# Optimization experiments

Hardware: AMD Instinct MI355X
Metric: run time of the kernel (lower is better)

Reference implementation:

```python
import jax, jax.numpy as jnp
import numpy as np


def sign_fn(x):
    # torch.sign(torch.sign(x) + 0.5): maps x >= 0 -> +1, x < 0 -> -1 (zero -> +1)
    return jnp.where(x >= 0, 1.0, -1.0).astype(x.dtype)


def setup_inputs() -> dict:
    key = jax.random.key(0)
    kx, kw, kb = jax.random.split(key, 3)
    TOKENS, IN, OUT = 8192, 4096, 4096
    x = jax.random.normal(kx, (TOKENS, IN), dtype=jnp.float32)
    weight = jax.random.normal(kw, (OUT, IN), dtype=jnp.float32)
    bias = jax.random.normal(kb, (OUT,), dtype=jnp.float32)
    return {"x": x, "weight": weight, "bias": bias}


def reference(x, weight, bias):
    b_weight = sign_fn(weight)  # [out, in], values in {+1, -1}
    b_bias = sign_fn(bias)      # [out]
    # nn.functional.linear: y = x @ W^T + b
    return jnp.einsum('ti,oi->to', x, b_weight) + b_bias
```

## Files before the change

### kernel.cpp

```cpp
#include <hip/hip_runtime.h>


typedef __attribute__((ext_vector_type(4))) int   i32x4;
typedef __attribute__((ext_vector_type(8))) short short8;
typedef __attribute__((ext_vector_type(4))) float f32x4;

constexpr int M = 8192;
constexpr int N = 4096;
constexpr int K = 4096;

constexpr int BM = 256, BN = 256, BK = 64;
constexpr int NTILES = K / BK;
constexpr int TILE_A = BM * BK;
constexpr int TILE_B = BN * BK;
constexpr int BUFSZ  = TILE_A + TILE_B;
constexpr int RING   = 4;

__device__ __forceinline__ void load_lds16(const void* g, void* l) {
    __builtin_amdgcn_global_load_lds(
        (const __attribute__((address_space(1))) unsigned int*)g,
        (__attribute__((address_space(3))) unsigned int*)l, 16, 0, 0);
}

constexpr int WB  = 1024;
constexpr int WCH = N * K / 8;

__global__ __launch_bounds__(256) void prep_fused(
    const float* __restrict__ X, const float* __restrict__ W,
    signed char* __restrict__ Xq, signed char* __restrict__ Wq,
    float* __restrict__ Scale) {
    __shared__ float wmax[4];
    const int t = threadIdx.x;

    if (blockIdx.x < M) {
        const int row = blockIdx.x;
        const float4* xr = reinterpret_cast<const float4*>(X + (size_t)row * K);
        float4 v[4];
        float mx = 0.f;
#pragma unroll
        for (int i = 0; i < 4; ++i) {
            v[i] = xr[t + i * 256];
            mx = fmaxf(mx, fmaxf(fmaxf(fabsf(v[i].x), fabsf(v[i].y)),
                                 fmaxf(fabsf(v[i].z), fabsf(v[i].w))));
        }
#pragma unroll
        for (int off = 32; off > 0; off >>= 1)
            mx = fmaxf(mx, __shfl_down(mx, off));
        if ((t & 63) == 0) wmax[t >> 6] = mx;
        __syncthreads();
        float rmax = fmaxf(fmaxf(wmax[0], wmax[1]), fmaxf(wmax[2], wmax[3]));
        rmax = fmaxf(rmax, 1e-20f);
        const float inv = 127.f / rmax;
        if (t == 0) Scale[row] = rmax * (1.f / 127.f);

        unsigned int* out = reinterpret_cast<unsigned int*>(Xq + (size_t)row * K);
#pragma unroll
        for (int i = 0; i < 4; ++i) {
            int q0 = (int)rintf(v[i].x * inv);
            int q1 = (int)rintf(v[i].y * inv);
            int q2 = (int)rintf(v[i].z * inv);
            int q3 = (int)rintf(v[i].w * inv);
            unsigned int p = (q0 & 255) | ((q1 & 255) << 8) |
                             ((q2 & 255) << 16) | ((unsigned)(q3 & 255) << 24);
            out[t + i * 256] = p;
        }
    } else {
        const float4* W4 = reinterpret_cast<const float4*>(W);
        uint2* O = reinterpret_cast<uint2*>(Wq);
        auto sg = [](float f) -> unsigned int { return (f >= 0.f) ? 1u : 0xFFu; };
        size_t idx = (size_t)(blockIdx.x - M) * 256 + t;
        const size_t stride = (size_t)WB * 256;
        for (size_t c = idx; c < (size_t)WCH; c += stride) {
            float4 a = W4[c * 2], b = W4[c * 2 + 1];
            uint2 o;
            o.x = sg(a.x) | (sg(a.y) << 8) | (sg(a.z) << 16) | (sg(a.w) << 24);
            o.y = sg(b.x) | (sg(b.y) << 8) | (sg(b.z) << 16) | (sg(b.w) << 24);
            O[c] = o;
        }
    }
}

struct GemmCtx {
    const signed char* Abase;
    const signed char* Bbase;
    int voff;
    signed char* lbase;
    unsigned baseA;
    unsigned baseB;
};

struct Frags { i32x4 b[4]; i32x4 a[8]; };

__device__ __forceinline__ void stage_full(const GemmCtx& c, int t) {
    signed char* d = c.lbase + (t & (RING - 1)) * BUFSZ;
    const size_t ko = (size_t)t * BK;
    load_lds16(c.Abase + ko + c.voff, d);
    load_lds16(c.Abase + (size_t)128 * K + ko + c.voff, d + 8192);
    load_lds16(c.Bbase + ko + c.voff, d + TILE_A);
    load_lds16(c.Bbase + (size_t)128 * K + ko + c.voff, d + TILE_A + 8192);
}

__device__ __forceinline__ void read_frags_asm(unsigned aA, unsigned aB,
                                               Frags& f) {
    asm volatile(
        "ds_read_b128 %0, %12 offset:0\n\t"
        "ds_read_b128 %1, %12 offset:1024\n\t"
        "ds_read_b128 %2, %12 offset:2048\n\t"
        "ds_read_b128 %3, %12 offset:3072\n\t"
        "ds_read_b128 %4, %13 offset:0\n\t"
        "ds_read_b128 %5, %13 offset:1024\n\t"
        "ds_read_b128 %6, %13 offset:2048\n\t"
        "ds_read_b128 %7, %13 offset:3072\n\t"
        "ds_read_b128 %8, %13 offset:4096\n\t"
        "ds_read_b128 %9, %13 offset:5120\n\t"
        "ds_read_b128 %10, %13 offset:6144\n\t"
        "ds_read_b128 %11, %13 offset:7168"
        : "=&v"(f.b[0]), "=&v"(f.b[1]), "=&v"(f.b[2]), "=&v"(f.b[3]),
          "=&v"(f.a[0]), "=&v"(f.a[1]), "=&v"(f.a[2]), "=&v"(f.a[3]),
          "=&v"(f.a[4]), "=&v"(f.a[5]), "=&v"(f.a[6]), "=&v"(f.a[7])
        : "v"(aB), "v"(aA));
}

__device__ __forceinline__ void do_mfma(const Frags& f, i32x4 (&acc)[8][4]) {
    __builtin_amdgcn_s_setprio(1);
#pragma unroll
    for (int mi = 0; mi < 8; ++mi)
#pragma unroll
        for (int ni = 0; ni < 4; ++ni)
            acc[mi][ni] = __builtin_amdgcn_mfma_i32_16x16x64_i8(
                f.a[mi], f.b[ni], acc[mi][ni], 0, 0, 0);
    __builtin_amdgcn_s_setprio(0);
}

template <int VM, bool STAGE, bool RDNEXT, bool BAR>
__device__ __forceinline__ void kstep(
    const GemmCtx& c, int j, Frags& cur, Frags& nxt, i32x4 (&acc)[8][4]) {
    if constexpr (RDNEXT) {
        const unsigned ring = (unsigned)(((j + 1) & (RING - 1)) * BUFSZ);
        read_frags_asm(c.baseA + ring, c.baseB + ring, nxt);
    }
    __builtin_amdgcn_sched_barrier(0);
    do_mfma(cur, acc);
    if constexpr (STAGE) stage_full(c, j + 4);
    if constexpr (VM >= 0)
        asm volatile("s_waitcnt vmcnt(%0)" :: "i"(VM) : "memory");
    asm volatile("s_waitcnt lgkmcnt(0)" ::: "memory");
    __builtin_amdgcn_sched_barrier(0);
    if constexpr (BAR) __builtin_amdgcn_s_barrier();
}

__global__ __launch_bounds__(512, 2) void gemm_i8_p(
    const signed char* __restrict__ Aq, const signed char* __restrict__ Bq,
    const float* __restrict__ Scale, const float* __restrict__ Bias,
    float* __restrict__ OUT) {
    __shared__ signed char smem[RING * BUFSZ];

    const int tid  = threadIdx.x;
    const int lane = tid & 63;
    const int w    = tid >> 6;
    const int wm   = w >> 2;
    const int wn   = w & 3;
    const int rl   = lane & 15;
    const int cq16 = (((lane >> 4) ^ ((rl >> 1) & 3)) << 4);

    const int wg  = blockIdx.x;
    const int lin = (wg & 7) * 64 + (wg >> 3);
    const int n0  = (lin & 15) * BN;
    const int m0  = (lin >> 4) * BM;

    const int srow = tid >> 2;
    const int cg   = ((tid & 3) ^ ((srow >> 1) & 3)) * 16;

    GemmCtx c;
    c.Abase = Aq + (size_t)m0 * K;
    c.Bbase = Bq + (size_t)n0 * K;
    c.voff  = srow * K + cg;
    c.lbase = smem + w * 1024;
    const unsigned lds0 = (unsigned)(unsigned long long)&smem[0];
    c.baseA = lds0 + (unsigned)((wm * 128 + rl) * BK + cq16);
    c.baseB = lds0 + (unsigned)(TILE_A + (wn * 64 + rl) * BK + cq16);

    i32x4 acc[8][4];
#pragma unroll
    for (int mi = 0; mi < 8; ++mi)
#pragma unroll
        for (int ni = 0; ni < 4; ++ni)
            acc[mi][ni] = (i32x4){0, 0, 0, 0};

    stage_full(c, 0); stage_full(c, 1); stage_full(c, 2); stage_full(c, 3);
    asm volatile("s_waitcnt vmcnt(8)" ::: "memory");
    __builtin_amdgcn_s_barrier();
    Frags fA, fB;
    read_frags_asm(c.baseA, c.baseB, fA);
    asm volatile("s_waitcnt lgkmcnt(0)" ::: "memory");
    __builtin_amdgcn_sched_barrier(0);
    __builtin_amdgcn_s_barrier();

    for (int j = 0; j < NTILES - 4; j += 2) {
        kstep<8, true, true, true>(c, j,     fA, fB, acc);
        kstep<8, true, true, true>(c, j + 1, fB, fA, acc);
    }
    kstep<4,  false, true,  true >(c, NTILES - 4, fA, fB, acc);
    kstep<0,  false, true,  true >(c, NTILES - 3, fB, fA, acc);
    kstep<-1, false, true,  false>(c, NTILES - 2, fA, fB, acc);
    kstep<-1, false, false, false>(c, NTILES - 1, fB, fA, acc);

#pragma unroll
    for (int ni = 0; ni < 4; ++ni) {
        const int gcol = n0 + wn * 64 + ni * 16 + rl;
        const float sb = (Bias[gcol] >= 0.f) ? 1.f : -1.f;
#pragma unroll
        for (int mi = 0; mi < 8; ++mi) {
            const int growb = m0 + wm * 128 + mi * 16 + (lane >> 4) * 4;
            const float4 sc = *reinterpret_cast<const float4*>(&Scale[growb]);
            OUT[(size_t)(growb + 0) * N + gcol] = (float)acc[mi][ni][0] * sc.x + sb;
            OUT[(size_t)(growb + 1) * N + gcol] = (float)acc[mi][ni][1] * sc.y + sb;
            OUT[(size_t)(growb + 2) * N + gcol] = (float)acc[mi][ni][2] * sc.z + sb;
            OUT[(size_t)(growb + 3) * N + gcol] = (float)acc[mi][ni][3] * sc.w + sb;
        }
    }
}

constexpr int MT   = 128;
constexpr int NTF  = 128;
constexpr int LDSS = 40;
constexpr int KTB  = 32;
__device__ __forceinline__ unsigned short f2b(float f) {
    unsigned int u = __builtin_bit_cast(unsigned int, f);
    u += 0x7FFFu + ((u >> 16) & 1u);
    return (unsigned short)(u >> 16);
}
__global__ __launch_bounds__(256) void binlin_fallback(
    const float* __restrict__ X, const float* __restrict__ W,
    const float* __restrict__ B, float* __restrict__ OUT) {
    __shared__ unsigned short As[MT][LDSS];
    __shared__ unsigned short Bs[NTF][LDSS];
    const int tid  = threadIdx.x;
    const int lane = tid & 63;
    const int wave = tid >> 6;
    const int wm   = wave >> 1;
    const int wn   = wave & 1;
    const int m0 = blockIdx.y * MT;
    const int n0 = blockIdx.x * NTF;
    const int rl = lane & 15;
    const int kq = (lane >> 4) * 8;
    f32x4 acc[4][4];
#pragma unroll
    for (int mi = 0; mi < 4; ++mi)
#pragma unroll
        for (int ni = 0; ni < 4; ++ni)
            acc[mi][ni] = (f32x4){0.f, 0.f, 0.f, 0.f};
    for (int k0 = 0; k0 < K; k0 += KTB) {
#pragma unroll
        for (int it = 0; it < 4; ++it) {
            int g = tid + it * 256, row = g >> 3, c4 = (g & 7) << 2;
            float4 v = *reinterpret_cast<const float4*>(&X[(size_t)(m0 + row) * K + k0 + c4]);
            ushort4 h;
            h.x = f2b(v.x); h.y = f2b(v.y); h.z = f2b(v.z); h.w = f2b(v.w);
            *reinterpret_cast<ushort4*>(&As[row][c4]) = h;
        }
#pragma unroll
        for (int it = 0; it < 4; ++it) {
            int g = tid + it * 256, row = g >> 3, c4 = (g & 7) << 2;
            float4 v = *reinterpret_cast<const float4*>(&W[(size_t)(n0 + row) * K + k0 + c4]);
            ushort4 h;
            h.x = (v.x >= 0.f) ? 0x3F80u : 0xBF80u;
            h.y = (v.y >= 0.f) ? 0x3F80u : 0xBF80u;
            h.z = (v.z >= 0.f) ? 0x3F80u : 0xBF80u;
            h.w = (v.w >= 0.f) ? 0x3F80u : 0xBF80u;
            *reinterpret_cast<ushort4*>(&Bs[row][c4]) = h;
        }
        __syncthreads();
        short8 a[4], b[4];
#pragma unroll
        for (int mi = 0; mi < 4; ++mi)
            a[mi] = *reinterpret_cast<const short8*>(&As[wm * 64 + mi * 16 + rl][kq]);
#pragma unroll
        for (int ni = 0; ni < 4; ++ni)
            b[ni] = *reinterpret_cast<const short8*>(&Bs[wn * 64 + ni * 16 + rl][kq]);
#pragma unroll
        for (int mi = 0; mi < 4; ++mi)
#pragma unroll
            for (int ni = 0; ni < 4; ++ni)
                acc[mi][ni] = __builtin_amdgcn_mfma_f32_16x16x32_bf16(
                    a[mi], b[ni], acc[mi][ni], 0, 0, 0);
        __syncthreads();
    }
#pragma unroll
    for (int ni = 0; ni < 4; ++ni) {
        int gcol = n0 + wn * 64 + ni * 16 + rl;
        float sb = (B[gcol] >= 0.f) ? 1.f : -1.f;
#pragma unroll
        for (int mi = 0; mi < 4; ++mi) {
            int growb = m0 + wm * 64 + mi * 16 + (lane >> 4) * 4;
#pragma unroll
            for (int r = 0; r < 4; ++r)
                OUT[(size_t)(growb + r) * N + gcol] = acc[mi][ni][r] + sb;
        }
    }
}

extern "C" void kernel_launch(void* const* d_in, const int* in_sizes, int n_in,
                              void* d_out, int out_size, void* d_ws, size_t ws_size,
                              hipStream_t stream) {
    const float* x  = (const float*)d_in[0];
    const float* w  = (const float*)d_in[1];
    const float* b  = (const float*)d_in[2];
    float* out      = (float*)d_out;

    const size_t need = (size_t)M * K + (size_t)N * K + (size_t)M * sizeof(float);
    if (ws_size >= need) {
        signed char* Xq = (signed char*)d_ws;
        signed char* Wq = Xq + (size_t)M * K;
        float* Scale    = (float*)(Wq + (size_t)N * K);

        prep_fused<<<dim3(M + WB), dim3(256), 0, stream>>>(x, w, Xq, Wq, Scale);
        gemm_i8_p<<<dim3((M / BM) * (N / BN)), dim3(512), 0, stream>>>(
            Xq, Wq, Scale, b, out);
    } else {
        dim3 grid(N / NTF, M / MT);
        binlin_fallback<<<grid, dim3(256), 0, stream>>>(x, w, b, out);
    }
}
```

Baseline: 402.5 us.

## Shrink GEMM tile to 128x256 with 4 waves and 3-slot LDS ring

Halves the M tile to 128 and uses 256-thread blocks (4 waves, each covering all 128 rows and 64 columns), doubling the grid. The LDS ring drops from 4 to 3 slots, and the pipeline is rewritten so global->LDS staging is issued at the start of each k-step with a full vmcnt(0) wait before the barrier. The smaller footprint aims at more resident blocks per CU and better load balance, at the cost of lower arithmetic intensity per block and a shallower prefetch depth.

```diff
diff --git a/kernel.cpp b/kernel.cpp
--- a/kernel.cpp
+++ b/kernel.cpp
@@ -9,12 +9,12 @@
 constexpr int N = 4096;
 constexpr int K = 4096;
 
-constexpr int BM = 256, BN = 256, BK = 64;
+constexpr int BM = 128, BN = 256, BK = 64;
 constexpr int NTILES = K / BK;
 constexpr int TILE_A = BM * BK;
 constexpr int TILE_B = BN * BK;
 constexpr int BUFSZ  = TILE_A + TILE_B;
-constexpr int RING   = 4;
+constexpr int RING   = 3;
 
 __device__ __forceinline__ void load_lds16(const void* g, void* l) {
     __builtin_amdgcn_global_load_lds(
@@ -91,13 +91,15 @@
 
 struct Frags { i32x4 b[4]; i32x4 a[8]; };
 
-__device__ __forceinline__ void stage_full(const GemmCtx& c, int t) {
-    signed char* d = c.lbase + (t & (RING - 1)) * BUFSZ;
+__device__ __forceinline__ void stage_full(const GemmCtx& c, int t, int slot) {
+    signed char* d = c.lbase + slot * BUFSZ;
     const size_t ko = (size_t)t * BK;
     load_lds16(c.Abase + ko + c.voff, d);
-    load_lds16(c.Abase + (size_t)128 * K + ko + c.voff, d + 8192);
+    load_lds16(c.Abase + (size_t)64 * K + ko + c.voff, d + 4096);
     load_lds16(c.Bbase + ko + c.voff, d + TILE_A);
+    load_lds16(c.Bbase + (size_t)64 * K + ko + c.voff, d + TILE_A + 4096);
     load_lds16(c.Bbase + (size_t)128 * K + ko + c.voff, d + TILE_A + 8192);
+    load_lds16(c.Bbase + (size_t)192 * K + ko + c.voff, d + TILE_A + 12288);
 }
 
 __device__ __forceinline__ void read_frags_asm(unsigned aA, unsigned aB,
@@ -132,24 +134,26 @@
     __builtin_amdgcn_s_setprio(0);
 }
 
-template <int VM, bool STAGE, bool RDNEXT, bool BAR>
+template <bool STAGE, bool RD, bool BAR>
 __device__ __forceinline__ void kstep(
-    const GemmCtx& c, int j, Frags& cur, Frags& nxt, i32x4 (&acc)[8][4]) {
-    if constexpr (RDNEXT) {
-        const unsigned ring = (unsigned)(((j + 1) & (RING - 1)) * BUFSZ);
+    const GemmCtx& c, int stage_t, int stage_slot, int rd_slot,
+    Frags& cur, Frags& nxt, i32x4 (&acc)[8][4]) {
+    if constexpr (STAGE) stage_full(c, stage_t, stage_slot);
+    if constexpr (RD) {
+        const unsigned ring = (unsigned)(rd_slot * BUFSZ);
         read_frags_asm(c.baseA + ring, c.baseB + ring, nxt);
     }
     __builtin_amdgcn_sched_barrier(0);
     do_mfma(cur, acc);
-    if constexpr (STAGE) stage_full(c, j + 4);
-    if constexpr (VM >= 0)
-        asm volatile("s_waitcnt vmcnt(%0)" :: "i"(VM) : "memory");
-    asm volatile("s_waitcnt lgkmcnt(0)" ::: "memory");
-    __builtin_amdgcn_sched_barrier(0);
-    if constexpr (BAR) __builtin_amdgcn_s_barrier();
-}
-
-__global__ __launch_bounds__(512, 2) void gemm_i8_p(
+    if constexpr (BAR) {
+        asm volatile("s_waitcnt vmcnt(0)" ::: "memory");
+        asm volatile("s_waitcnt lgkmcnt(0)" ::: "memory");
+        __builtin_amdgcn_sched_barrier(0);
+        __builtin_amdgcn_s_barrier();
+    }
+}
+
+__global__ __launch_bounds__(256, 2) void gemm_i8_p(
     const signed char* __restrict__ Aq, const signed char* __restrict__ Bq,
     const float* __restrict__ Scale, const float* __restrict__ Bias,
     float* __restrict__ OUT) {
@@ -158,13 +162,12 @@
     const int tid  = threadIdx.x;
     const int lane = tid & 63;
     const int w    = tid >> 6;
-    const int wm   = w >> 2;
-    const int wn   = w & 3;
+    const int wn   = w;
     const int rl   = lane & 15;
     const int cq16 = (((lane >> 4) ^ ((rl >> 1) & 3)) << 4);
 
     const int wg  = blockIdx.x;
-    const int lin = (wg & 7) * 64 + (wg >> 3);
+    const int lin = (wg & 7) * 128 + (wg >> 3);
     const int n0  = (lin & 15) * BN;
     const int m0  = (lin >> 4) * BM;
 
@@ -177,7 +180,7 @@
     c.voff  = srow * K + cg;
     c.lbase = smem + w * 1024;
     const unsigned lds0 = (unsigned)(unsigned long long)&smem[0];
-    c.baseA = lds0 + (unsigned)((wm * 128 + rl) * BK + cq16);
+    c.baseA = lds0 + (unsigned)(rl * BK + cq16);
     c.baseB = lds0 + (unsigned)(TILE_A + (wn * 64 + rl) * BK + cq16);
 
     i32x4 acc[8][4];
@@ -187,23 +190,28 @@
         for (int ni = 0; ni < 4; ++ni)
             acc[mi][ni] = (i32x4){0, 0, 0, 0};
 
-    stage_full(c, 0); stage_full(c, 1); stage_full(c, 2); stage_full(c, 3);
-    asm volatile("s_waitcnt vmcnt(8)" ::: "memory");
+    stage_full(c, 0, 0); stage_full(c, 1, 1);
+    asm volatile("s_waitcnt vmcnt(6)" ::: "memory");
     __builtin_amdgcn_s_barrier();
     Frags fA, fB;
     read_frags_asm(c.baseA, c.baseB, fA);
+    asm volatile("s_waitcnt vmcnt(0)" ::: "memory");
     asm volatile("s_waitcnt lgkmcnt(0)" ::: "memory");
     __builtin_amdgcn_sched_barrier(0);
     __builtin_amdgcn_s_barrier();
 
-    for (int j = 0; j < NTILES - 4; j += 2) {
-        kstep<8, true, true, true>(c, j,     fA, fB, acc);
-        kstep<8, true, true, true>(c, j + 1, fB, fA, acc);
-    }
-    kstep<4,  false, true,  true >(c, NTILES - 4, fA, fB, acc);
-    kstep<0,  false, true,  true >(c, NTILES - 3, fB, fA, acc);
-    kstep<-1, false, true,  false>(c, NTILES - 2, fA, fB, acc);
-    kstep<-1, false, false, false>(c, NTILES - 1, fB, fA, acc);
+    for (int jb = 0; jb < 60; jb += 6) {
+        kstep<true, true, true>(c, jb + 2, 2, 1, fA, fB, acc);
+        kstep<true, true, true>(c, jb + 3, 0, 2, fB, fA, acc);
+        kstep<true, true, true>(c, jb + 4, 1, 0, fA, fB, acc);
+        kstep<true, true, true>(c, jb + 5, 2, 1, fB, fA, acc);
+        kstep<true, true, true>(c, jb + 6, 0, 2, fA, fB, acc);
+        kstep<true, true, true>(c, jb + 7, 1, 0, fB, fA, acc);
+    }
+    kstep<true,  true,  true >(c, 62, 2, 1, fA, fB, acc);
+    kstep<true,  true,  true >(c, 63, 0, 2, fB, fA, acc);
+    kstep<false, true,  true >(c, 0,  0, 0, fA, fB, acc);
+    kstep<false, false, false>(c, 0,  0, 0, fB, fA, acc);
 
 #pragma unroll
     for (int ni = 0; ni < 4; ++ni) {
@@ -211,7 +219,7 @@
         const float sb = (Bias[gcol] >= 0.f) ? 1.f : -1.f;
 #pragma unroll
         for (int mi = 0; mi < 8; ++mi) {
-            const int growb = m0 + wm * 128 + mi * 16 + (lane >> 4) * 4;
+            const int growb = m0 + mi * 16 + (lane >> 4) * 4;
             const float4 sc = *reinterpret_cast<const float4*>(&Scale[growb]);
             OUT[(size_t)(growb + 0) * N + gcol] = (float)acc[mi][ni][0] * sc.x + sb;
             OUT[(size_t)(growb + 1) * N + gcol] = (float)acc[mi][ni][1] * sc.y + sb;
@@ -315,7 +323,7 @@
         float* Scale    = (float*)(Wq + (size_t)N * K);
 
         prep_fused<<<dim3(M + WB), dim3(256), 0, stream>>>(x, w, Xq, Wq, Scale);
-        gemm_i8_p<<<dim3((M / BM) * (N / BN)), dim3(512), 0, stream>>>(
+        gemm_i8_p<<<dim3((M / BM) * (N / BN)), dim3(256), 0, stream>>>(
             Xq, Wq, Scale, b, out);
     } else {
         dim3 grid(N / NTF, M / MT);
```

Result: slower. 423.0 us (+5.1%).
